# Kernel optimization log

Measured on AMD Instinct MI355X. Metric: run time of the kernel, lower is better.

The kernel has to match this reference:

```python
import jax, jax.numpy as jnp
import numpy as np

B, S, D_IN = 4, 2048, 1024
EMBED, H = 1024, 16
HD = EMBED // H  # 64


def setup_inputs() -> dict:
    key = jax.random.key(0)
    k1, k2, k3 = jax.random.split(key, 3)
    x = jax.random.normal(k1, (B, S, D_IN), dtype=jnp.float32)
    # xavier_uniform for torch Linear weight [out, in]
    lim_qkv = float(np.sqrt(6.0 / (D_IN + 3 * EMBED)))
    W_qkv = jax.random.uniform(k2, (3 * EMBED, D_IN), minval=-lim_qkv, maxval=lim_qkv, dtype=jnp.float32)
    b_qkv = jnp.zeros((3 * EMBED,), dtype=jnp.float32)
    lim_o = float(np.sqrt(6.0 / (EMBED + EMBED)))
    W_out = jax.random.uniform(k3, (EMBED, EMBED), minval=-lim_o, maxval=lim_o, dtype=jnp.float32)
    b_out = jnp.zeros((EMBED,), dtype=jnp.float32)
    return {"x": x, "W_qkv": W_qkv, "b_qkv": b_qkv, "W_out": W_out, "b_out": b_out}


def reference(x, W_qkv, b_qkv, W_out, b_out):
    b, s, _ = x.shape
    qkv = x @ W_qkv.T + b_qkv                      # [b, s, 3*embed]
    # einops 'b s (h c d) -> c b h s d': fused dim groups as (h, 3, d)
    qkv = qkv.reshape(b, s, H, 3, HD)
    qkv = jnp.transpose(qkv, (3, 0, 2, 1, 4))      # [3, b, h, s, d]
    q, k, v = qkv[0], qkv[1], qkv[2]
    scale = 1.0 / jnp.sqrt(jnp.asarray(HD, dtype=q.dtype))
    logits = jnp.einsum('bhqd,bhkd->bhqk', q, k) * scale
    attn = jax.nn.softmax(logits, axis=-1)
    vals = jnp.einsum('bhqk,bhkd->bhqd', attn, v)  # [b, h, s, d]
    vals = jnp.transpose(vals, (0, 2, 1, 3)).reshape(b, s, EMBED)
    return vals @ W_out.T + b_out
```

## Files before the change

### kernel.cpp

```cpp
#include <hip/hip_runtime.h>
#include <hip/hip_bf16.h>
#include <stdint.h>

#define B_   4
#define S_   2048
#define DIN  1024
#define EMB  1024
#define H_   16
#define HD_  64
#define TOK  (B_*S_)
#define NQKV 3072

using bf16  = __hip_bfloat16;
using f32x4 = __attribute__((ext_vector_type(4))) float;
using f32x16 = __attribute__((ext_vector_type(16))) float;
using s16x8 = __attribute__((ext_vector_type(8))) short;
using bf16x8 = __attribute__((ext_vector_type(8))) __bf16;

__device__ __forceinline__ f32x4 mfma16(s16x8 a, s16x8 b, f32x4 c) {
  return __builtin_amdgcn_mfma_f32_16x16x32_bf16(
      __builtin_bit_cast(bf16x8, a), __builtin_bit_cast(bf16x8, b), c, 0, 0, 0);
}
__device__ __forceinline__ f32x16 mfma32(s16x8 a, s16x8 b, f32x16 c) {
  return __builtin_amdgcn_mfma_f32_32x32x16_bf16(
      __builtin_bit_cast(bf16x8, a), __builtin_bit_cast(bf16x8, b), c, 0, 0, 0);
}

__device__ __forceinline__ void gload_lds16(const void* g, void* l) {
  __builtin_amdgcn_global_load_lds(
      (const __attribute__((address_space(1))) uint32_t*)g,
      (__attribute__((address_space(3))) uint32_t*)l, 16, 0, 0);
}

__device__ __forceinline__ uint32_t cvtpk_bf16(float lo, float hi) {
  uint32_t r;
  asm("v_cvt_pk_bf16_f32 %0, %1, %2" : "=v"(r) : "v"(lo), "v"(hi));
  return r;
}
__device__ __forceinline__ void plswap32(uint32_t &a, uint32_t &b) {
  asm("v_permlane32_swap_b32 %0, %1" : "+v"(a), "+v"(b));
}

union U8 { s16x8 v; bf16 b[8]; };
union PaU { uint32_t w[4]; s16x8 v; };

__global__ __launch_bounds__(256) void cvt_all(const float* __restrict__ x,
                                               const float* __restrict__ wqkv,
                                               const float* __restrict__ wout,
                                               bf16* __restrict__ xb,
                                               bf16* __restrict__ wqkvb,
                                               bf16* __restrict__ woutb) {
  int b = blockIdx.x;
  const float* in; bf16* out; int base;
  if (b < 4096)      { in = x;    out = xb;    base = b; }
  else if (b < 5632) { in = wqkv; out = wqkvb; base = b - 4096; }
  else               { in = wout; out = woutb; base = b - 5632; }
  int i = (base * 256 + (int)threadIdx.x) * 8;
  float4 a = *(const float4*)(in + i);
  float4 c = *(const float4*)(in + i + 4);
  U8 u;
  u.b[0] = __float2bfloat16(a.x); u.b[1] = __float2bfloat16(a.y);
  u.b[2] = __float2bfloat16(a.z); u.b[3] = __float2bfloat16(a.w);
  u.b[4] = __float2bfloat16(c.x); u.b[5] = __float2bfloat16(c.y);
  u.b[6] = __float2bfloat16(c.z); u.b[7] = __float2bfloat16(c.w);
  *(s16x8*)(out + i) = u.v;
}

template<int MODE>
__global__ __launch_bounds__(256) void gemm_bt(
    const bf16* __restrict__ A, const bf16* __restrict__ Bw,
    const float* __restrict__ bias,
    bf16* __restrict__ outQK, bf16* __restrict__ outV,
    float* __restrict__ outF, int N, int K)
{
  const int tid  = threadIdx.x;
  const int lane = tid & 63;
  const int w    = tid >> 6;
  const int wm   = w >> 1, wn = w & 1;
  const int bn0  = blockIdx.x * 128;
  const int bm0  = blockIdx.y * 128;

  __shared__ __align__(16) bf16 As[128 * 64];
  __shared__ __align__(16) bf16 Bs[128 * 64];

  f32x4 acc[4][4];
  const f32x4 zero = {0.f, 0.f, 0.f, 0.f};
  for (int mt = 0; mt < 4; ++mt)
    for (int nt = 0; nt < 4; ++nt) acc[mt][nt] = zero;

  for (int kt = 0; kt < K; kt += 64) {
    for (int i = 0; i < 4; ++i) {
      int c   = i * 256 + tid;
      int row = c >> 3, p = c & 7;
      int sc  = p ^ (row & 7);
      gload_lds16(A + (size_t)(bm0 + row) * K + kt + sc * 8, (char*)As + c * 16);
      gload_lds16(Bw + (size_t)(bn0 + row) * K + kt + sc * 8, (char*)Bs + c * 16);
    }
    __syncthreads();

    s16x8 af[4][2], bfr[4][2];
    for (int mt = 0; mt < 4; ++mt)
      for (int kk = 0; kk < 2; ++kk) {
        int row  = wm * 64 + mt * 16 + (lane & 15);
        int byte = row * 128 + (((kk * 4 + (lane >> 4)) ^ (row & 7)) << 4);
        af[mt][kk] = *(const s16x8*)((const char*)As + byte);
      }
    for (int nt = 0; nt < 4; ++nt)
      for (int kk = 0; kk < 2; ++kk) {
        int row  = wn * 64 + nt * 16 + (lane & 15);
        int byte = row * 128 + (((kk * 4 + (lane >> 4)) ^ (row & 7)) << 4);
        bfr[nt][kk] = *(const s16x8*)((const char*)Bs + byte);
      }
    for (int kk = 0; kk < 2; ++kk)
      for (int mt = 0; mt < 4; ++mt)
        for (int nt = 0; nt < 4; ++nt)
          acc[mt][nt] = mfma16(af[mt][kk], bfr[nt][kk], acc[mt][nt]);
    __syncthreads();
  }

  const int col_l = lane & 15;
  const int rgrp  = lane >> 4;
  for (int mt = 0; mt < 4; ++mt)
    for (int nt = 0; nt < 4; ++nt) {
      int n0  = bn0 + wn * 64 + nt * 16;
      int col = n0 + col_l;
      float bv = bias[col];
      if (MODE == 0) {
        int h = col / 192, rem = col % 192;
        int cc = rem / 64, d = rem % 64;
        for (int r = 0; r < 4; ++r) {
          int row = bm0 + wm * 64 + mt * 16 + rgrp * 4 + r;
          bf16 bvv = __float2bfloat16(acc[mt][nt][r] + bv);
          if (cc == 2) {
            int bb = row >> 11, s = row & 2047;
            outV[(((size_t)bb * H_ + h) * HD_ + d) * S_ + s] = bvv;
          } else {
            outQK[(size_t)row * NQKV + col] = bvv;
          }
        }
      } else {
        for (int r = 0; r < 4; ++r) {
          int row = bm0 + wm * 64 + mt * 16 + rgrp * 4 + r;
          outF[(size_t)row * EMB + col] = acc[mt][nt][r] + bv;
        }
      }
    }
}

__global__ __launch_bounds__(512, 2) void attn2(const bf16* __restrict__ qkvb,
                                                const bf16* __restrict__ vb,
                                                bf16* __restrict__ ob)
{
  const int tid = threadIdx.x, lane = tid & 63, w = tid >> 6;
  const int hi = lane >> 5, l31 = lane & 31;
  const int f  = blockIdx.x;
  const int bh = (f & 7) | (((f >> 6) & 7) << 3);
  const int qt = (f >> 3) & 7;
  const int bb = bh >> 4, h = bh & 15;
  const int q0 = qt * 256;
  const size_t tokbase = (size_t)bb * S_;

  __shared__ __align__(16) bf16 Ks[2][64 * 64];
  __shared__ __align__(16) bf16 Vts[2][64 * 64];

  s16x8 qf[4];
  {
    const int qrow = q0 + w * 32 + l31;
    const bf16* qp = qkvb + (tokbase + qrow) * NQKV + h * 192 + hi * 8;
    #pragma unroll
    for (int ks = 0; ks < 4; ++ks) {
      U8 u; u.v = *(const s16x8*)(qp + ks * 16);
      #pragma unroll
      for (int j = 0; j < 8; ++j)
        u.b[j] = __float2bfloat16(__bfloat162float(u.b[j]) * 0.18033688011112042f);
      qf[ks] = u.v;
    }
  }

  f32x16 zero16;
  #pragma unroll
  for (int i = 0; i < 16; ++i) zero16[i] = 0.f;
  f32x16 oA = zero16, oB = zero16;
  f32x16 nm16 = zero16;
  float l0 = 0.f;

  const bf16* Kbase = qkvb + tokbase * NQKV + h * 192 + 64;
  const bf16* Vbase = vb + (size_t)bh * HD_ * S_;

  auto STAGE = [&](int b, int t) {
    const int kv0 = t * 64;
    const int c = tid;
    const int k8 = c >> 6, kv = c & 63;
    gload_lds16(Kbase + (size_t)(kv0 + kv) * NQKV + k8 * 8,
                (char*)Ks[b] + c * 16);
    const int ch = c >> 6, d = c & 63;
    gload_lds16(Vbase + (size_t)d * S_ + kv0 + ch * 8,
                (char*)Vts[b] + c * 16);
  };

  STAGE(0, 0);
  __syncthreads();

  int cur = 0;
  for (int t = 0; t < S_ / 64; ++t) {
    if (t < S_ / 64 - 1) STAGE(cur ^ 1, t + 1);

    f32x16 pA, pB;
    #pragma unroll
    for (int ks = 0; ks < 4; ++ks) {
      const char* kb = (const char*)Ks[cur] + (2 * ks + hi) * 1024;
      {
        s16x8 kf = *(const s16x8*)(kb + l31 * 16);
        pA = mfma32(kf, qf[ks], ks == 0 ? nm16 : pA);
      }
      {
        s16x8 kf = *(const s16x8*)(kb + 512 + l31 * 16);
        pB = mfma32(kf, qf[ks], ks == 0 ? nm16 : pB);
      }
    }

    float mx8[8];
    #pragma unroll
    for (int i = 0; i < 8; ++i)
      mx8[i] = fmaxf(fmaxf(pA[i], pA[i + 8]), fmaxf(pB[i], pB[i + 8]));
    float pmax = fmaxf(fmaxf(fmaxf(mx8[0], mx8[4]), fmaxf(mx8[1], mx8[5])),
                       fmaxf(fmaxf(mx8[2], mx8[6]), fmaxf(mx8[3], mx8[7])));
    pmax = fmaxf(pmax, __shfl_xor(pmax, 32));

    if (__any(pmax > 11.0f)) {
      float al = __builtin_amdgcn_exp2f(-pmax);
      l0 *= al;
      #pragma unroll
      for (int r = 0; r < 16; ++r) {
        float alr = __shfl(al, (r & 3) + 8 * (r >> 2) + 4 * hi);
        oA[r] *= alr; oB[r] *= alr;
      }
      #pragma unroll
      for (int r = 0; r < 16; ++r) { pA[r] -= pmax; pB[r] -= pmax; }
      #pragma unroll
      for (int i = 0; i < 16; ++i) nm16[i] -= pmax;
    }

    #pragma unroll
    for (int r = 0; r < 16; ++r) {
      pA[r] = __builtin_amdgcn_exp2f(pA[r]);
      pB[r] = __builtin_amdgcn_exp2f(pB[r]);
    }
    float s8[8];
    #pragma unroll
    for (int i = 0; i < 8; ++i)
      s8[i] = (pA[i] + pA[i + 8]) + (pB[i] + pB[i + 8]);
    l0 += ((s8[0] + s8[1]) + (s8[2] + s8[3])) +
          ((s8[4] + s8[5]) + (s8[6] + s8[7]));

    #pragma unroll
    for (int s = 0; s < 4; ++s) {
      const int sub = s & 1;
      const f32x16 &ph = (s < 2) ? pA : pB;
      uint32_t L0 = cvtpk_bf16(ph[8 * sub + 0], ph[8 * sub + 1]);
      uint32_t L1 = cvtpk_bf16(ph[8 * sub + 2], ph[8 * sub + 3]);
      uint32_t H0 = cvtpk_bf16(ph[8 * sub + 4], ph[8 * sub + 5]);
      uint32_t H1 = cvtpk_bf16(ph[8 * sub + 6], ph[8 * sub + 7]);
      plswap32(L0, H0);
      plswap32(L1, H1);
      PaU pa; pa.w[0] = L0; pa.w[1] = L1; pa.w[2] = H0; pa.w[3] = H1;
      const char* vbp = (const char*)Vts[cur] + (2 * s + hi) * 1024;
      {
        s16x8 vf = *(const s16x8*)(vbp + l31 * 16);
        oA = mfma32(pa.v, vf, oA);
      }
      {
        s16x8 vf = *(const s16x8*)(vbp + 512 + l31 * 16);
        oB = mfma32(pa.v, vf, oB);
      }
    }
    __syncthreads();
    cur ^= 1;
  }

  float l0t = l0 + __shfl_xor(l0, 32);
  float inv = 1.0f / l0t;
  #pragma unroll
  for (int r = 0; r < 16; ++r) {
    int q = (r & 3) + 8 * (r >> 2) + 4 * hi;
    float invr = __shfl(inv, q);
    int qrow = q0 + w * 32 + q;
    bf16* op = ob + (tokbase + qrow) * EMB + h * 64 + l31;
    op[0]  = __float2bfloat16(oA[r] * invr);
    op[32] = __float2bfloat16(oB[r] * invr);
  }
}

extern "C" void kernel_launch(void* const* d_in, const int* in_sizes, int n_in,
                              void* d_out, int out_size, void* d_ws, size_t ws_size,
                              hipStream_t stream) {
  const float* x    = (const float*)d_in[0];
  const float* Wqkv = (const float*)d_in[1];
  const float* bqkv = (const float*)d_in[2];
  const float* Wout = (const float*)d_in[3];
  const float* bout = (const float*)d_in[4];
  float* out = (float*)d_out;

  char* ws = (char*)d_ws;
  bf16* xb    = (bf16*)(ws);
  bf16* wqkvb = (bf16*)(ws + 16777216);
  bf16* woutb = (bf16*)(ws + 23068672);
  bf16* qkvb  = (bf16*)(ws + 25165824);
  bf16* vb    = (bf16*)(ws + 75497472);
  bf16* ob    = xb;

  cvt_all<<<dim3(6144), 256, 0, stream>>>(x, Wqkv, Wout, xb, wqkvb, woutb);

  gemm_bt<0><<<dim3(NQKV / 128, TOK / 128), 256, 0, stream>>>(
      xb, wqkvb, bqkv, qkvb, vb, nullptr, NQKV, DIN);

  attn2<<<dim3(512), 512, 0, stream>>>(qkvb, vb, ob);

  gemm_bt<1><<<dim3(EMB / 128, TOK / 128), 256, 0, stream>>>(
      ob, woutb, bout, nullptr, nullptr, out, EMB, EMB);
}
```

Baseline: 222.4 us.

## Stage K/V tiles through registers into padded LDS instead of direct global-to-LDS loads

```diff
diff --git a/kernel.cpp b/kernel.cpp
--- a/kernel.cpp
+++ b/kernel.cpp
@@ -160,8 +160,8 @@
   const int q0 = qt * 256;
   const size_t tokbase = (size_t)bb * S_;
 
-  __shared__ __align__(16) bf16 Ks[2][64 * 64];
-  __shared__ __align__(16) bf16 Vts[2][64 * 64];
+  __shared__ __align__(16) char KsB[2][8 * 1040];
+  __shared__ __align__(16) char VtsB[2][8 * 1040];
 
   s16x8 qf[4];
   {
@@ -187,28 +187,33 @@
   const bf16* Kbase = qkvb + tokbase * NQKV + h * 192 + 64;
   const bf16* Vbase = vb + (size_t)bh * HD_ * S_;
 
-  auto STAGE = [&](int b, int t) {
-    const int kv0 = t * 64;
-    const int c = tid;
-    const int k8 = c >> 6, kv = c & 63;
-    gload_lds16(Kbase + (size_t)(kv0 + kv) * NQKV + k8 * 8,
-                (char*)Ks[b] + c * 16);
-    const int ch = c >> 6, d = c & 63;
-    gload_lds16(Vbase + (size_t)d * S_ + kv0 + ch * 8,
-                (char*)Vts[b] + c * 16);
+  const int srow = tid >> 3, sp = tid & 7;
+  const bf16* kSrc = Kbase + (size_t)srow * NQKV + sp * 8;
+  const bf16* vSrc = Vbase + (size_t)srow * S_ + sp * 8;
+  const int   sByte = sp * 1040 + srow * 16;
+
+  s16x8 kreg, vreg;
+  auto LOAD = [&](int t) {
+    kreg = *(const s16x8*)(kSrc + (size_t)t * 64 * NQKV);
+    vreg = *(const s16x8*)(vSrc + (size_t)t * 64);
   };
-
-  STAGE(0, 0);
+  auto WRITE = [&](int b) {
+    *(s16x8*)(KsB[b] + sByte) = kreg;
+    *(s16x8*)(VtsB[b] + sByte) = vreg;
+  };
+
+  LOAD(0);
+  WRITE(0);
   __syncthreads();
 
   int cur = 0;
   for (int t = 0; t < S_ / 64; ++t) {
-    if (t < S_ / 64 - 1) STAGE(cur ^ 1, t + 1);
+    if (t < S_ / 64 - 1) LOAD(t + 1);
 
     f32x16 pA, pB;
     #pragma unroll
     for (int ks = 0; ks < 4; ++ks) {
-      const char* kb = (const char*)Ks[cur] + (2 * ks + hi) * 1024;
+      const char* kb = KsB[cur] + (2 * ks + hi) * 1040;
       {
         s16x8 kf = *(const s16x8*)(kb + l31 * 16);
         pA = mfma32(kf, qf[ks], ks == 0 ? nm16 : pA);
@@ -264,7 +269,7 @@
       plswap32(L0, H0);
       plswap32(L1, H1);
       PaU pa; pa.w[0] = L0; pa.w[1] = L1; pa.w[2] = H0; pa.w[3] = H1;
-      const char* vbp = (const char*)Vts[cur] + (2 * s + hi) * 1024;
+      const char* vbp = VtsB[cur] + (2 * s + hi) * 1040;
       {
         s16x8 vf = *(const s16x8*)(vbp + l31 * 16);
         oA = mfma32(pa.v, vf, oA);
@@ -274,6 +279,8 @@
         oB = mfma32(pa.v, vf, oB);
       }
     }
+
+    if (t < S_ / 64 - 1) WRITE(cur ^ 1);
     __syncthreads();
     cur ^= 1;
   }
```

Measured after the change: 204.3 us. 8.1% less time.
